# Performance work log

Hardware: AMD Instinct MI355X
Metric: run time of the kernel (lower is better)

Reference implementation:

```python
import jax, jax.numpy as jnp
import numpy as np

B, DIRS, C, H, W = 2, 64, 630, 128, 128

def setup_inputs() -> dict:
    key = jax.random.key(0)
    k1, k2, k3, k4, k5 = jax.random.split(key, 5)
    theta_global = jax.random.normal(k1, (B, 4, H, W), dtype=jnp.float32) * 0.1
    theta_dir = jax.random.normal(k2, (B, DIRS, 6, H, W), dtype=jnp.float32) * 0.1
    t_vec = jax.random.uniform(k3, (C,), dtype=jnp.float32)
    b_vec = jax.random.uniform(k4, (C,), dtype=jnp.float32)
    P = jax.random.normal(k5, (C, DIRS), dtype=jnp.float32) * 0.1
    return {"theta_global": theta_global, "theta_dir": theta_dir,
            "t_vec": t_vec, "b_vec": b_vec, "P": P}

def _log_s(theta_global, theta_dir, t_vec, b_vec, P):
    ln_s0 = theta_global[:, 0:1]   # [B,1,H,W]
    r = theta_global[:, 1:2]
    sigma20 = theta_global[:, 2:3]
    sigma30 = theta_global[:, 3:4]
    # project all six direction-coefficient maps at once: [B,6,C,H,W]
    proj = jnp.einsum('cd,bdkhw->bkchw', P, theta_dir)
    D_ch, s11, s02, s21, s12, s03 = (proj[:, k] for k in range(6))
    t = t_vec.reshape(1, -1, 1, 1)  # [1,C,1,1]
    b = b_vec.reshape(1, -1, 1, 1)
    t2, b2, tb = t * t, b * b, t * b
    t3, b3, t2b, tb2 = t2 * t, b2 * b, t2 * b, t * b2
    log_s = (ln_s0 - r * t - D_ch * b
             + 0.5 * (sigma20 * t2 + 2.0 * s11 * tb + s02 * b2)
             - (1.0 / 6.0) * (sigma30 * t3 + 3.0 * s21 * t2b + 3.0 * s12 * tb2 + s03 * b3))
    return log_s

def reference(theta_global, theta_dir, t_vec, b_vec, P):
    return jnp.exp(_log_s(theta_global, theta_dir, t_vec, b_vec, P))
```

## Files before the change

kernel.cpp:

```cpp
#include <hip/hip_runtime.h>
#include <math.h>

#define BATCH 2
#define NDIRS 64
#define NCH   630
#define MPAD  640
#define HW    16384
#define KDIR  384
#define NT    12
#define PANEL 128
#define NPOSW 5
#define NITER (NPOSW * NT)
#define BROWE 392

#define BS_OFF 0
#define TV_OFF 100352
#define TG_OFF 102912
#define LDS_TOTAL 104960

typedef float f32x4 __attribute__((ext_vector_type(4)));
typedef short s16x8 __attribute__((ext_vector_type(8)));

__device__ __forceinline__ ushort f2bf(float f) {
    unsigned u = __builtin_bit_cast(unsigned, f);
    u = (u + 0x7FFFu + ((u >> 16) & 1u)) >> 16;
    return (ushort)u;
}

__device__ __forceinline__ uint cvt_pk_bf16(float lo, float hi) {
    uint r;
    asm("v_cvt_pk_bf16_f32 %0, %1, %2" : "=v"(r) : "v"(lo), "v"(hi));
    return r;
}

__device__ __forceinline__ f32x4 ntload(const float* p) {
    return __builtin_nontemporal_load((const f32x4*)p);
}

__global__ void prep_kernel(const float* __restrict__ t_vec,
                            const float* __restrict__ b_vec,
                            const float* __restrict__ P,
                            ushort* __restrict__ W2b) {
    int c = blockIdx.x;
    int j = threadIdx.x;
    float w = 0.0f;
    if (c < NCH) {
        int d = j / 6, k = j - d * 6;
        float t = t_vec[c];
        float bb = b_vec[c];
        float coeff;
        switch (k) {
            case 0:  coeff = -bb;                           break;
            case 1:  coeff = t * bb;                        break;
            case 2:  coeff = 0.5f * bb * bb;                break;
            case 3:  coeff = -0.5f * t * t * bb;            break;
            case 4:  coeff = -0.5f * t * bb * bb;           break;
            default: coeff = -(1.0f / 6.0f) * bb * bb * bb; break;
        }
        w = coeff * P[c * NDIRS + d];
    }
    int kstep = j >> 5, k5 = j & 31, k8 = k5 >> 3, klo = k5 & 7;
    int s = k8 ^ ((c >> 1) & 3);
    W2b[c * KDIR + kstep * 32 + s * 8 + klo] = f2bf(w);
}

__global__ __launch_bounds__(512, 2) void fused_gemm(
        const ushort* __restrict__ W2b,
        const float*  __restrict__ TD,
        const float*  __restrict__ t_vec,
        const float*  __restrict__ TG,
        float* __restrict__ out)
{
    extern __shared__ char lds[];

    const int nt_ = blockIdx.x;
    const int bz  = blockIdx.y;
    const int n0  = nt_ * PANEL;

    const int tid  = threadIdx.x;
    const int lane = tid & 63;
    const int wv   = tid >> 6;
    const int mg   = wv & 3;
    const int w    = wv >> 2;
    const int l15 = lane & 15, lhi = lane >> 4;
    const int aslot = lhi ^ ((l15 >> 1) & 3);

    ushort* bsU = (ushort*)(lds + BS_OFF);
    float*  tvl = (float*)(lds + TV_OFF);
    float*  tgl = (float*)(lds + TG_OFF);

    tvl[tid] = t_vec[tid];
    if (tid < NCH - 512) tvl[tid + 512] = t_vec[tid + 512];
    else if (tid + 512 < MPAD) tvl[tid + 512] = 0.0f;
    {
        int p = tid >> 7, px = tid & 127;
        tgl[p * PANEL + px] = TG[((size_t)bz * 4 + p) * HW + n0 + px];
    }

    const ushort* aP = W2b + (mg * 160 + l15) * KDIR + aslot * 8;
    s16x8 afb[3][2];
    afb[0][0] = *(const s16x8*)(aP);
    afb[0][1] = *(const s16x8*)(aP + 16 * KDIR);
    afb[1][0] = *(const s16x8*)(aP + 32);
    afb[1][1] = *(const s16x8*)(aP + 16 * KDIR + 32);
    __builtin_amdgcn_sched_barrier(0);

    const int kq2 = mg * 4 + lhi;
    const int pg  = w * 16 + l15;
    const float* bR = TD + ((size_t)bz * KDIR + 2 * kq2) * HW + n0 + pg * 4;
    const int sxor = ((kq2 >> 2) ^ (pg & 3) ^ ((pg >> 2) & 3)) & 3;
    const int wbase = (kq2 & 3) * 2;

    {
        f32x4 lo0, hi0, lo1, hi1, lo2, hi2, lo3, hi3;
        lo0 = ntload(bR);
        hi0 = ntload(bR + HW);
        lo1 = ntload(bR + (size_t)32 * HW);
        hi1 = ntload(bR + (size_t)33 * HW);
        lo2 = ntload(bR + (size_t)64 * HW);
        hi2 = ntload(bR + (size_t)65 * HW);

#define BSTEP(S, LC, HC, LN, HN)                                               \
        {                                                                      \
            if ((S) + 3 < NT) {                                                \
                LN = ntload(bR + (size_t)(((S) + 3) * 32) * HW);               \
                HN = ntload(bR + (size_t)(((S) + 3) * 32 + 1) * HW);           \
            }                                                                  \
            _Pragma("unroll")                                                  \
            for (int i = 0; i < 4; ++i) {                                      \
                uint w_ = cvt_pk_bf16(LC[i], HC[i]);                           \
                int s_ = (sxor ^ i) & 3;                                       \
                *(uint*)&bsU[(pg * 4 + i) * BROWE + (S) * 32 + s_ * 8 + wbase] = w_; \
            }                                                                  \
        }
        BSTEP(0, lo0, hi0, lo3, hi3)  BSTEP(1, lo1, hi1, lo0, hi0)
        BSTEP(2, lo2, hi2, lo1, hi1)  BSTEP(3, lo3, hi3, lo2, hi2)
        BSTEP(4, lo0, hi0, lo3, hi3)  BSTEP(5, lo1, hi1, lo0, hi0)
        BSTEP(6, lo2, hi2, lo1, hi1)  BSTEP(7, lo3, hi3, lo2, hi2)
        BSTEP(8, lo0, hi0, lo3, hi3)  BSTEP(9, lo1, hi1, lo0, hi0)
        BSTEP(10, lo2, hi2, lo1, hi1) BSTEP(11, lo3, hi3, lo2, hi2)
#undef BSTEP
    }

    asm volatile("s_waitcnt lgkmcnt(0)" ::: "memory");
    __builtin_amdgcn_s_barrier();
    __builtin_amdgcn_sched_barrier(0);

    float gg[4][4];
    #pragma unroll
    for (int n = 0; n < 4; ++n)
        #pragma unroll
        for (int p = 0; p < 4; ++p)
            gg[n][p] = tgl[p * PANEL + w * 64 + n * 16 + l15];

    f32x4 acc[2][4];
    #pragma unroll
    for (int m = 0; m < 2; ++m)
        #pragma unroll
        for (int n = 0; n < 4; ++n) acc[m][n] = (f32x4){0.f, 0.f, 0.f, 0.f};

#define ITER(G)                                                                \
    {                                                                          \
        constexpr int T_ = (G) % NT, buf_ = (G) % 3;                           \
        constexpr int gn_ = (G) + 2;                                           \
        if constexpr (gn_ < NITER) {                                           \
            constexpr int pi_ = gn_ / NT, ti_ = gn_ % NT, nb_ = gn_ % 3;       \
            afb[nb_][0] = *(const s16x8*)(aP + (pi_ * 32) * KDIR + ti_ * 32);  \
            afb[nb_][1] = *(const s16x8*)(aP + (pi_ * 32 + 16) * KDIR          \
                                          + ti_ * 32);                         \
            __builtin_amdgcn_sched_barrier(0);                                 \
        }                                                                      \
        s16x8 bf[4];                                                           \
        _Pragma("unroll")                                                      \
        for (int n = 0; n < 4; ++n) {                                          \
            const int rs_ = (lhi ^ (l15 & 3) ^ ((l15 >> 2) & 3) ^ (n)) & 3;    \
            bf[n] = *(const s16x8*)&bsU[(w * 64 + n * 16 + l15) * BROWE        \
                                        + T_ * 32 + rs_ * 8];                  \
        }                                                                      \
        __builtin_amdgcn_s_setprio(1);                                         \
        _Pragma("unroll")                                                      \
        for (int m = 0; m < 2; ++m)                                            \
            _Pragma("unroll")                                                  \
            for (int n = 0; n < 4; ++n)                                        \
                acc[m][n] = __builtin_amdgcn_mfma_f32_16x16x32_bf16(           \
                                afb[buf_][m], bf[n], acc[m][n], 0, 0, 0);      \
        __builtin_amdgcn_s_setprio(0);                                         \
    }

#define EPI(P_)                                                                \
    {                                                                          \
        _Pragma("unroll")                                                      \
        for (int m = 0; m < 2; ++m) {                                          \
            _Pragma("unroll")                                                  \
            for (int r = 0; r < 4; ++r) {                                      \
                int c = mg * 160 + (P_) * 32 + m * 16 + lhi * 4 + r;           \
                float t_ = tvl[c];                                             \
                float ct1 = -t_, ct2 = 0.5f * t_ * t_;                         \
                float ct3 = -(1.0f / 6.0f) * t_ * t_ * t_;                     \
                float* orow = out + ((size_t)bz * NCH + c) * HW + n0           \
                              + w * 64 + l15;                                  \
                _Pragma("unroll")                                              \
                for (int n = 0; n < 4; ++n) {                                  \
                    float base = gg[n][0] + ct1 * gg[n][1]                     \
                               + ct2 * gg[n][2] + ct3 * gg[n][3];              \
                    __builtin_nontemporal_store(                               \
                        __expf(acc[m][n][r] + base), orow + n * 16);           \
                }                                                              \
            }                                                                  \
        }                                                                      \
        _Pragma("unroll")                                                      \
        for (int m = 0; m < 2; ++m)                                            \
            _Pragma("unroll")                                                  \
            for (int n = 0; n < 4; ++n) acc[m][n] = (f32x4){0.f,0.f,0.f,0.f};  \
    }

    ITER(0)  ITER(1)  ITER(2)  ITER(3)  ITER(4)  ITER(5)
    ITER(6)  ITER(7)  ITER(8)  ITER(9)  ITER(10) ITER(11)
    EPI(0)
    ITER(12) ITER(13) ITER(14) ITER(15) ITER(16) ITER(17)
    ITER(18) ITER(19) ITER(20) ITER(21) ITER(22) ITER(23)
    EPI(1)
    ITER(24) ITER(25) ITER(26) ITER(27) ITER(28) ITER(29)
    ITER(30) ITER(31) ITER(32) ITER(33) ITER(34) ITER(35)
    EPI(2)
    ITER(36) ITER(37) ITER(38) ITER(39) ITER(40) ITER(41)
    ITER(42) ITER(43) ITER(44) ITER(45) ITER(46) ITER(47)
    EPI(3)
    ITER(48) ITER(49) ITER(50) ITER(51) ITER(52) ITER(53)
    ITER(54) ITER(55) ITER(56) ITER(57) ITER(58) ITER(59)

    {
        #pragma unroll
        for (int m = 0; m < 2; ++m) {
            #pragma unroll
            for (int r = 0; r < 4; ++r) {
                int c = mg * 160 + 4 * 32 + m * 16 + lhi * 4 + r;
                if (c < NCH) {
                    float t_ = tvl[c];
                    float ct1 = -t_, ct2 = 0.5f * t_ * t_;
                    float ct3 = -(1.0f / 6.0f) * t_ * t_ * t_;
                    float* orow = out + ((size_t)bz * NCH + c) * HW + n0
                                  + w * 64 + l15;
                    #pragma unroll
                    for (int n = 0; n < 4; ++n) {
                        float base = gg[n][0] + ct1 * gg[n][1]
                                   + ct2 * gg[n][2] + ct3 * gg[n][3];
                        __builtin_nontemporal_store(
                            __expf(acc[m][n][r] + base), orow + n * 16);
                    }
                }
            }
        }
    }

#undef EPI
#undef ITER
}

extern "C" void kernel_launch(void* const* d_in, const int* in_sizes, int n_in,
                              void* d_out, int out_size, void* d_ws, size_t ws_size,
                              hipStream_t stream) {
    const float* theta_global = (const float*)d_in[0];
    const float* theta_dir    = (const float*)d_in[1];
    const float* t_vec        = (const float*)d_in[2];
    const float* b_vec        = (const float*)d_in[3];
    const float* P            = (const float*)d_in[4];
    float* out = (float*)d_out;

    ushort* W2b = (ushort*)d_ws;

    (void)hipFuncSetAttribute((const void*)fused_gemm,
                              hipFuncAttributeMaxDynamicSharedMemorySize,
                              LDS_TOTAL);

    prep_kernel<<<dim3(MPAD), dim3(KDIR), 0, stream>>>(t_vec, b_vec, P, W2b);
    fused_gemm<<<dim3(HW / PANEL, BATCH), 512, LDS_TOTAL, stream>>>(
        W2b, theta_dir, t_vec, theta_global, out);
}
```

Before: 37.55 us.

## Interleave B-panel staging into LDS with the first position's MFMA iterations

Instead of converting and writing all 12 K-slices of the theta_dir panel to LDS before any compute, each K-slice is now staged and followed by the MFMA iteration that consumes the previous slice, with a barrier after each step. The aim is to overlap global loads and bf16 conversion of the B panel with matrix math for the first output position, hiding the load prologue. The cost is eleven extra workgroup barriers and tighter coupling between load latency and compute in the first phase.

```diff
diff --git a/kernel.cpp b/kernel.cpp
--- a/kernel.cpp
+++ b/kernel.cpp
@@ -111,47 +111,32 @@
     const int sxor = ((kq2 >> 2) ^ (pg & 3) ^ ((pg >> 2) & 3)) & 3;
     const int wbase = (kq2 & 3) * 2;
 
-    {
-        f32x4 lo0, hi0, lo1, hi1, lo2, hi2, lo3, hi3;
-        lo0 = ntload(bR);
-        hi0 = ntload(bR + HW);
-        lo1 = ntload(bR + (size_t)32 * HW);
-        hi1 = ntload(bR + (size_t)33 * HW);
-        lo2 = ntload(bR + (size_t)64 * HW);
-        hi2 = ntload(bR + (size_t)65 * HW);
-
-#define BSTEP(S, LC, HC, LN, HN)                                               \
-        {                                                                      \
-            if ((S) + 3 < NT) {                                                \
-                LN = ntload(bR + (size_t)(((S) + 3) * 32) * HW);               \
-                HN = ntload(bR + (size_t)(((S) + 3) * 32 + 1) * HW);           \
-            }                                                                  \
-            _Pragma("unroll")                                                  \
-            for (int i = 0; i < 4; ++i) {                                      \
-                uint w_ = cvt_pk_bf16(LC[i], HC[i]);                           \
-                int s_ = (sxor ^ i) & 3;                                       \
-                *(uint*)&bsU[(pg * 4 + i) * BROWE + (S) * 32 + s_ * 8 + wbase] = w_; \
-            }                                                                  \
-        }
-        BSTEP(0, lo0, hi0, lo3, hi3)  BSTEP(1, lo1, hi1, lo0, hi0)
-        BSTEP(2, lo2, hi2, lo1, hi1)  BSTEP(3, lo3, hi3, lo2, hi2)
-        BSTEP(4, lo0, hi0, lo3, hi3)  BSTEP(5, lo1, hi1, lo0, hi0)
-        BSTEP(6, lo2, hi2, lo1, hi1)  BSTEP(7, lo3, hi3, lo2, hi2)
-        BSTEP(8, lo0, hi0, lo3, hi3)  BSTEP(9, lo1, hi1, lo0, hi0)
-        BSTEP(10, lo2, hi2, lo1, hi1) BSTEP(11, lo3, hi3, lo2, hi2)
-#undef BSTEP
-    }
-
-    asm volatile("s_waitcnt lgkmcnt(0)" ::: "memory");
-    __builtin_amdgcn_s_barrier();
+    f32x4 lo0, hi0, lo1, hi1, lo2, hi2, lo3, hi3;
+    lo0 = ntload(bR);
+    hi0 = ntload(bR + HW);
+    lo1 = ntload(bR + (size_t)32 * HW);
+    hi1 = ntload(bR + (size_t)33 * HW);
+    lo2 = ntload(bR + (size_t)64 * HW);
+    hi2 = ntload(bR + (size_t)65 * HW);
+
+#define BST(S, LC, HC, LN, HN)                                                 \
+    {                                                                          \
+        if ((S) + 3 < NT) {                                                    \
+            LN = ntload(bR + (size_t)(((S) + 3) * 32) * HW);                   \
+            HN = ntload(bR + (size_t)(((S) + 3) * 32 + 1) * HW);               \
+        }                                                                      \
+        _Pragma("unroll")                                                      \
+        for (int i = 0; i < 4; ++i) {                                          \
+            uint w_ = cvt_pk_bf16(LC[i], HC[i]);                               \
+            int s_ = (sxor ^ i) & 3;                                           \
+            *(uint*)&bsU[(pg * 4 + i) * BROWE + (S) * 32 + s_ * 8 + wbase] = w_; \
+        }                                                                      \
+    }
+
+#define SYNC()                                                                 \
+    asm volatile("s_waitcnt lgkmcnt(0)" ::: "memory");                         \
+    __builtin_amdgcn_s_barrier();                                              \
     __builtin_amdgcn_sched_barrier(0);
-
-    float gg[4][4];
-    #pragma unroll
-    for (int n = 0; n < 4; ++n)
-        #pragma unroll
-        for (int p = 0; p < 4; ++p)
-            gg[n][p] = tgl[p * PANEL + w * 64 + n * 16 + l15];
 
     f32x4 acc[2][4];
     #pragma unroll
@@ -214,9 +199,30 @@
             for (int n = 0; n < 4; ++n) acc[m][n] = (f32x4){0.f,0.f,0.f,0.f};  \
     }
 
-    ITER(0)  ITER(1)  ITER(2)  ITER(3)  ITER(4)  ITER(5)
-    ITER(6)  ITER(7)  ITER(8)  ITER(9)  ITER(10) ITER(11)
+    BST(0, lo0, hi0, lo3, hi3)
+    SYNC()
+
+    float gg[4][4];
+    #pragma unroll
+    for (int n = 0; n < 4; ++n)
+        #pragma unroll
+        for (int p = 0; p < 4; ++p)
+            gg[n][p] = tgl[p * PANEL + w * 64 + n * 16 + l15];
+
+    BST(1,  lo1, hi1, lo0, hi0)  ITER(0)  SYNC()
+    BST(2,  lo2, hi2, lo1, hi1)  ITER(1)  SYNC()
+    BST(3,  lo3, hi3, lo2, hi2)  ITER(2)  SYNC()
+    BST(4,  lo0, hi0, lo3, hi3)  ITER(3)  SYNC()
+    BST(5,  lo1, hi1, lo0, hi0)  ITER(4)  SYNC()
+    BST(6,  lo2, hi2, lo1, hi1)  ITER(5)  SYNC()
+    BST(7,  lo3, hi3, lo2, hi2)  ITER(6)  SYNC()
+    BST(8,  lo0, hi0, lo3, hi3)  ITER(7)  SYNC()
+    BST(9,  lo1, hi1, lo0, hi0)  ITER(8)  SYNC()
+    BST(10, lo2, hi2, lo1, hi1)  ITER(9)  SYNC()
+    BST(11, lo3, hi3, lo2, hi2)  ITER(10) SYNC()
+    ITER(11)
     EPI(0)
+
     ITER(12) ITER(13) ITER(14) ITER(15) ITER(16) ITER(17)
     ITER(18) ITER(19) ITER(20) ITER(21) ITER(22) ITER(23)
     EPI(1)
@@ -255,6 +261,8 @@
 
 #undef EPI
 #undef ITER
+#undef SYNC
+#undef BST
 }
 
 extern "C" void kernel_launch(void* const* d_in, const int* in_sizes, int n_in,
```

New measurement: 38.25 us. About the same (+1.9%).

## Fuse coefficient-weight prep into GEMM, building bf16 A fragments on the fly

Applied to the files above, without the earlier changes.

Removes the separate prep kernel that wrote a bf16 weight matrix to workspace. Each wave now reads P rows and t/b values directly, computes the per-channel polynomial coefficients, scales and packs them to bf16 inside the MFMA loop. The K dimension is reordered to coefficient-major (k-index = coeff*64+dir), and the theta_dir load offsets are changed to match. This saves one kernel launch and a workspace round-trip. The cost is extra fp32 global loads and VALU conversion work in every block, which is 256 blocks recomputing the same weights.

```diff
diff --git a/kernel.cpp b/kernel.cpp
--- a/kernel.cpp
+++ b/kernel.cpp
@@ -20,12 +20,7 @@
 
 typedef float f32x4 __attribute__((ext_vector_type(4)));
 typedef short s16x8 __attribute__((ext_vector_type(8)));
-
-__device__ __forceinline__ ushort f2bf(float f) {
-    unsigned u = __builtin_bit_cast(unsigned, f);
-    u = (u + 0x7FFFu + ((u >> 16) & 1u)) >> 16;
-    return (ushort)u;
-}
+typedef uint  u32x4 __attribute__((ext_vector_type(4)));
 
 __device__ __forceinline__ uint cvt_pk_bf16(float lo, float hi) {
     uint r;
@@ -37,38 +32,12 @@
     return __builtin_nontemporal_load((const f32x4*)p);
 }
 
-__global__ void prep_kernel(const float* __restrict__ t_vec,
-                            const float* __restrict__ b_vec,
-                            const float* __restrict__ P,
-                            ushort* __restrict__ W2b) {
-    int c = blockIdx.x;
-    int j = threadIdx.x;
-    float w = 0.0f;
-    if (c < NCH) {
-        int d = j / 6, k = j - d * 6;
-        float t = t_vec[c];
-        float bb = b_vec[c];
-        float coeff;
-        switch (k) {
-            case 0:  coeff = -bb;                           break;
-            case 1:  coeff = t * bb;                        break;
-            case 2:  coeff = 0.5f * bb * bb;                break;
-            case 3:  coeff = -0.5f * t * t * bb;            break;
-            case 4:  coeff = -0.5f * t * bb * bb;           break;
-            default: coeff = -(1.0f / 6.0f) * bb * bb * bb; break;
-        }
-        w = coeff * P[c * NDIRS + d];
-    }
-    int kstep = j >> 5, k5 = j & 31, k8 = k5 >> 3, klo = k5 & 7;
-    int s = k8 ^ ((c >> 1) & 3);
-    W2b[c * KDIR + kstep * 32 + s * 8 + klo] = f2bf(w);
-}
-
 __global__ __launch_bounds__(512, 2) void fused_gemm(
-        const ushort* __restrict__ W2b,
-        const float*  __restrict__ TD,
-        const float*  __restrict__ t_vec,
-        const float*  __restrict__ TG,
+        const float* __restrict__ P,
+        const float* __restrict__ TD,
+        const float* __restrict__ t_vec,
+        const float* __restrict__ b_vec,
+        const float* __restrict__ TG,
         float* __restrict__ out)
 {
     extern __shared__ char lds[];
@@ -83,7 +52,7 @@
     const int mg   = wv & 3;
     const int w    = wv >> 2;
     const int l15 = lane & 15, lhi = lane >> 4;
-    const int aslot = lhi ^ ((l15 >> 1) & 3);
+    const int lhi8 = lhi << 3;
 
     ushort* bsU = (ushort*)(lds + BS_OFF);
     float*  tvl = (float*)(lds + TV_OFF);
@@ -97,34 +66,79 @@
         tgl[p * PANEL + px] = TG[((size_t)bz * 4 + p) * HW + n0 + px];
     }
 
-    const ushort* aP = W2b + (mg * 160 + l15) * KDIR + aslot * 8;
+    float cfA[6], cfB[6];
+    const float *pA0, *pA1;
+
+#define COEF(P_)                                                               \
+    {                                                                          \
+        int c0_ = mg * 160 + (P_) * 32 + l15;                                  \
+        int cA_ = (c0_ < NCH) ? c0_ : (NCH - 1);                               \
+        int cB_ = (c0_ + 16 < NCH) ? (c0_ + 16) : (NCH - 1);                   \
+        float t0_ = t_vec[cA_], b0_ = b_vec[cA_];                              \
+        float t1_ = t_vec[cB_], b1_ = b_vec[cB_];                              \
+        cfA[0] = -b0_;                     cfB[0] = -b1_;                      \
+        cfA[1] = t0_ * b0_;                cfB[1] = t1_ * b1_;                 \
+        cfA[2] = 0.5f * b0_ * b0_;         cfB[2] = 0.5f * b1_ * b1_;          \
+        cfA[3] = -0.5f * t0_ * t0_ * b0_;  cfB[3] = -0.5f * t1_ * t1_ * b1_;   \
+        cfA[4] = -0.5f * t0_ * b0_ * b0_;  cfB[4] = -0.5f * t1_ * b1_ * b1_;   \
+        cfA[5] = -(1.0f/6.0f) * b0_ * b0_ * b0_;                               \
+        cfB[5] = -(1.0f/6.0f) * b1_ * b1_ * b1_;                               \
+        pA0 = P + cA_ * 64;                                                    \
+        pA1 = P + cB_ * 64;                                                    \
+    }
+
     s16x8 afb[3][2];
-    afb[0][0] = *(const s16x8*)(aP);
-    afb[0][1] = *(const s16x8*)(aP + 16 * KDIR);
-    afb[1][0] = *(const s16x8*)(aP + 32);
-    afb[1][1] = *(const s16x8*)(aP + 16 * KDIR + 32);
+
+#define AFINIT(NB_, TI_)                                                       \
+    {                                                                          \
+        constexpr int kk_ = (TI_) >> 1;                                        \
+        const int d0_ = (((TI_) & 1) << 5) + lhi8;                             \
+        f32x4 qa0_ = *(const f32x4*)(pA0 + d0_);                               \
+        f32x4 qa1_ = *(const f32x4*)(pA0 + d0_ + 4);                           \
+        f32x4 qb0_ = *(const f32x4*)(pA1 + d0_);                               \
+        f32x4 qb1_ = *(const f32x4*)(pA1 + d0_ + 4);                           \
+        float ca_ = cfA[kk_], cb_ = cfB[kk_];                                  \
+        u32x4 ua_, ub_;                                                        \
+        ua_[0] = cvt_pk_bf16(ca_*qa0_[0], ca_*qa0_[1]);                        \
+        ua_[1] = cvt_pk_bf16(ca_*qa0_[2], ca_*qa0_[3]);                        \
+        ua_[2] = cvt_pk_bf16(ca_*qa1_[0], ca_*qa1_[1]);                        \
+        ua_[3] = cvt_pk_bf16(ca_*qa1_[2], ca_*qa1_[3]);                        \
+        ub_[0] = cvt_pk_bf16(cb_*qb0_[0], cb_*qb0_[1]);                        \
+        ub_[1] = cvt_pk_bf16(cb_*qb0_[2], cb_*qb0_[3]);                        \
+        ub_[2] = cvt_pk_bf16(cb_*qb1_[0], cb_*qb1_[1]);                        \
+        ub_[3] = cvt_pk_bf16(cb_*qb1_[2], cb_*qb1_[3]);                        \
+        afb[NB_][0] = __builtin_bit_cast(s16x8, ua_);                          \
+        afb[NB_][1] = __builtin_bit_cast(s16x8, ub_);                          \
+    }
+
+    COEF(0)
+    AFINIT(0, 0)
+    AFINIT(1, 1)
     __builtin_amdgcn_sched_barrier(0);
 
     const int kq2 = mg * 4 + lhi;
     const int pg  = w * 16 + l15;
-    const float* bR = TD + ((size_t)bz * KDIR + 2 * kq2) * HW + n0 + pg * 4;
+    const float* bT = TD + (size_t)bz * KDIR * HW + (size_t)(12 * kq2) * HW
+                      + n0 + pg * 4;
     const int sxor = ((kq2 >> 2) ^ (pg & 3) ^ ((pg >> 2) & 3)) & 3;
     const int wbase = (kq2 & 3) * 2;
 
+#define BOFF(S) ((size_t)((((S) & 1) * 192) + ((S) >> 1)) * HW)
+
     {
         f32x4 lo0, hi0, lo1, hi1, lo2, hi2, lo3, hi3;
-        lo0 = ntload(bR);
-        hi0 = ntload(bR + HW);
-        lo1 = ntload(bR + (size_t)32 * HW);
-        hi1 = ntload(bR + (size_t)33 * HW);
-        lo2 = ntload(bR + (size_t)64 * HW);
-        hi2 = ntload(bR + (size_t)65 * HW);
+        lo0 = ntload(bT + BOFF(0));
+        hi0 = ntload(bT + BOFF(0) + 6 * HW);
+        lo1 = ntload(bT + BOFF(1));
+        hi1 = ntload(bT + BOFF(1) + 6 * HW);
+        lo2 = ntload(bT + BOFF(2));
+        hi2 = ntload(bT + BOFF(2) + 6 * HW);
 
 #define BSTEP(S, LC, HC, LN, HN)                                               \
         {                                                                      \
             if ((S) + 3 < NT) {                                                \
-                LN = ntload(bR + (size_t)(((S) + 3) * 32) * HW);               \
-                HN = ntload(bR + (size_t)(((S) + 3) * 32 + 1) * HW);           \
+                LN = ntload(bT + BOFF((S) + 3));                               \
+                HN = ntload(bT + BOFF((S) + 3) + 6 * HW);                      \
             }                                                                  \
             _Pragma("unroll")                                                  \
             for (int i = 0; i < 4; ++i) {                                      \
@@ -163,11 +177,15 @@
     {                                                                          \
         constexpr int T_ = (G) % NT, buf_ = (G) % 3;                           \
         constexpr int gn_ = (G) + 2;                                           \
+        constexpr int ti_ = gn_ % NT, nb_ = gn_ % 3;                           \
+        constexpr int kk_ = ti_ >> 1;                                          \
+        f32x4 qa0_, qa1_, qb0_, qb1_;                                          \
         if constexpr (gn_ < NITER) {                                           \
-            constexpr int pi_ = gn_ / NT, ti_ = gn_ % NT, nb_ = gn_ % 3;       \
-            afb[nb_][0] = *(const s16x8*)(aP + (pi_ * 32) * KDIR + ti_ * 32);  \
-            afb[nb_][1] = *(const s16x8*)(aP + (pi_ * 32 + 16) * KDIR          \
-                                          + ti_ * 32);                         \
+            const int d0_ = ((ti_ & 1) << 5) + lhi8;                           \
+            qa0_ = *(const f32x4*)(pA0 + d0_);                                 \
+            qa1_ = *(const f32x4*)(pA0 + d0_ + 4);                             \
+            qb0_ = *(const f32x4*)(pA1 + d0_);                                 \
+            qb1_ = *(const f32x4*)(pA1 + d0_ + 4);                             \
             __builtin_amdgcn_sched_barrier(0);                                 \
         }                                                                      \
         s16x8 bf[4];                                                           \
@@ -185,6 +203,21 @@
                 acc[m][n] = __builtin_amdgcn_mfma_f32_16x16x32_bf16(           \
                                 afb[buf_][m], bf[n], acc[m][n], 0, 0, 0);      \
         __builtin_amdgcn_s_setprio(0);                                         \
+        __builtin_amdgcn_sched_barrier(0);                                     \
+        if constexpr (gn_ < NITER) {                                           \
+            float ca_ = cfA[kk_], cb_ = cfB[kk_];                              \
+            u32x4 ua_, ub_;                                                    \
+            ua_[0] = cvt_pk_bf16(ca_*qa0_[0], ca_*qa0_[1]);                    \
+            ua_[1] = cvt_pk_bf16(ca_*qa0_[2], ca_*qa0_[3]);                    \
+            ua_[2] = cvt_pk_bf16(ca_*qa1_[0], ca_*qa1_[1]);                    \
+            ua_[3] = cvt_pk_bf16(ca_*qa1_[2], ca_*qa1_[3]);                    \
+            ub_[0] = cvt_pk_bf16(cb_*qb0_[0], cb_*qb0_[1]);                    \
+            ub_[1] = cvt_pk_bf16(cb_*qb0_[2], cb_*qb0_[3]);                    \
+            ub_[2] = cvt_pk_bf16(cb_*qb1_[0], cb_*qb1_[1]);                    \
+            ub_[3] = cvt_pk_bf16(cb_*qb1_[2], cb_*qb1_[3]);                    \
+            afb[nb_][0] = __builtin_bit_cast(s16x8, ua_);                      \
+            afb[nb_][1] = __builtin_bit_cast(s16x8, ub_);                      \
+        }                                                                      \
     }
 
 #define EPI(P_)                                                                \
@@ -215,16 +248,24 @@
     }
 
     ITER(0)  ITER(1)  ITER(2)  ITER(3)  ITER(4)  ITER(5)
-    ITER(6)  ITER(7)  ITER(8)  ITER(9)  ITER(10) ITER(11)
+    ITER(6)  ITER(7)  ITER(8)  ITER(9)
+    COEF(1)
+    ITER(10) ITER(11)
     EPI(0)
     ITER(12) ITER(13) ITER(14) ITER(15) ITER(16) ITER(17)
-    ITER(18) ITER(19) ITER(20) ITER(21) ITER(22) ITER(23)
+    ITER(18) ITER(19) ITER(20) ITER(21)
+    COEF(2)
+    ITER(22) ITER(23)
     EPI(1)
     ITER(24) ITER(25) ITER(26) ITER(27) ITER(28) ITER(29)
-    ITER(30) ITER(31) ITER(32) ITER(33) ITER(34) ITER(35)
+    ITER(30) ITER(31) ITER(32) ITER(33)
+    COEF(3)
+    ITER(34) ITER(35)
     EPI(2)
     ITER(36) ITER(37) ITER(38) ITER(39) ITER(40) ITER(41)
-    ITER(42) ITER(43) ITER(44) ITER(45) ITER(46) ITER(47)
+    ITER(42) ITER(43) ITER(44) ITER(45)
+    COEF(4)
+    ITER(46) ITER(47)
     EPI(3)
     ITER(48) ITER(49) ITER(50) ITER(51) ITER(52) ITER(53)
     ITER(54) ITER(55) ITER(56) ITER(57) ITER(58) ITER(59)
@@ -255,6 +296,9 @@
 
 #undef EPI
 #undef ITER
+#undef AFINIT
+#undef COEF
+#undef BOFF
 }
 
 extern "C" void kernel_launch(void* const* d_in, const int* in_sizes, int n_in,
@@ -267,13 +311,12 @@
     const float* P            = (const float*)d_in[4];
     float* out = (float*)d_out;
 
-    ushort* W2b = (ushort*)d_ws;
+    (void)d_ws; (void)ws_size;
 
     (void)hipFuncSetAttribute((const void*)fused_gemm,
                               hipFuncAttributeMaxDynamicSharedMemorySize,
                               LDS_TOTAL);
 
-    prep_kernel<<<dim3(MPAD), dim3(KDIR), 0, stream>>>(t_vec, b_vec, P, W2b);
     fused_gemm<<<dim3(HW / PANEL, BATCH), 512, LDS_TOTAL, stream>>>(
-        W2b, theta_dir, t_vec, theta_global, out);
+        P, theta_dir, t_vec, b_vec, theta_global, out);
 }
```

After: 66.59 us. 77.3% more time.
